# Performance work log

Hardware: AMD Instinct MI355X
Metric: run time of the kernel (lower is better)

Reference implementation:

```python
import jax, jax.numpy as jnp
import numpy as np

EPS = 0.01
H = 256
W = 256
C = 3
RADIUS_PX = 1.5          # splat radius in pixels
K_PPP = 8                # points_per_pixel
RAD_POW = 2
TAU = 1                  # accumulation_tau
WIN = 5                  # 5x5 candidate pixel window per point (covers radius 1.5)


def make_xyzs():
    # matches torch buffer: rows are (x, y, 1, 1) over flattened (H, W)
    xs = jnp.arange(W, dtype=jnp.float32)
    ys = jnp.arange(H, dtype=jnp.float32)
    X, Y = jnp.meshgrid(xs, ys)  # (H, W), X varies along width
    ones = jnp.ones_like(X)
    return jnp.stack([X, Y, ones, ones], 0).reshape(1, 4, H * W)


def project_pts(pred_pts, Kmat, K_inv, RT_cam1, RTinv_cam2):
    # pred_pts: (bs, 1, N) depths
    xyzs = make_xyzs()
    proj = xyzs * pred_pts                       # (bs, 4, N)
    proj = proj.at[:, 3, :].set(1.0)
    cam1 = jnp.einsum('bij,bjn->bin', K_inv, proj)
    wrld = jnp.einsum('bij,bjn->bin', RT_cam1, cam1)
    newc = jnp.einsum('bij,bjn->bin', RTinv_cam2, wrld)
    xy = jnp.einsum('bij,bjn->bin', Kmat, newc)
    z = xy[:, 2:3]
    mask = jnp.abs(z) < EPS
    zs = jnp.where(mask, EPS, z)
    sx = xy[:, 0:1] / zs / float(W - 1) * 2.0 - 1.0
    sy = xy[:, 1:2] / zs / float(H - 1) * 2.0 - 1.0
    sampler = jnp.concatenate([sx, sy, z], 1)    # (bs, 3, N)
    sampler = jnp.where(mask, -10.0, sampler)
    return sampler


def splat_one(pts, alpha_pts, feats):
    # pts: (N,3) ndc x,y + depth z; alpha_pts: (N,); feats: (C,N)
    N = pts.shape[0]
    x = (pts[:, 0] + 1.0) * 0.5 * (W - 1)        # ndc -> pixel coords
    y = (pts[:, 1] + 1.0) * 0.5 * (H - 1)
    z = pts[:, 2]
    radius_ndc = RADIUS_PX / float(W) * 2.0
    px0 = jnp.floor(x).astype(jnp.int32)
    py0 = jnp.floor(y).astype(jnp.int32)
    offs = jnp.arange(WIN, dtype=jnp.int32) - WIN // 2
    oy, ox = jnp.meshgrid(offs, offs, indexing='ij')
    oy = oy.reshape(-1)
    ox = ox.reshape(-1)                           # (25,)
    py = py0[:, None] + oy[None, :]               # (N, 25)
    px = px0[:, None] + ox[None, :]
    d2_pix = (px.astype(jnp.float32) - x[:, None]) ** 2 + (py.astype(jnp.float32) - y[:, None]) ** 2
    inb = (px >= 0) & (px < W) & (py >= 0) & (py < H)
    valid = inb & (d2_pix <= RADIUS_PX ** 2) & (z[:, None] > 0.0)
    d2_ndc = d2_pix * (2.0 / float(W)) ** 2
    dist_norm = d2_ndc / (radius_ndc ** RAD_POW)
    a = (1.0 - jnp.sqrt(jnp.clip(dist_norm, 1e-3, 1.0))) ** TAU
    a = a * alpha_pts[:, None]
    a = jnp.where(valid, a, 0.0)
    pix = jnp.where(valid, py * W + px, H * W)    # invalid -> dump segment
    M = N * WIN * WIN
    pixf = pix.reshape(M)
    zf = jnp.broadcast_to(z[:, None], pix.shape).reshape(M)
    af = a.reshape(M)
    ptid = jnp.broadcast_to(jnp.arange(N, dtype=jnp.int32)[:, None], pix.shape).reshape(M)
    # depth-ordered z-buffer: sort by (pixel, z), keep first K per pixel
    order = jnp.lexsort((zf, pixf))
    pixs = pixf[order]
    as_ = af[order]
    ids = ptid[order]
    first = jnp.searchsorted(pixs, pixs, side='left')
    rank = jnp.arange(M) - first
    keep = (rank < K_PPP) & (pixs < H * W)
    slot = jnp.where(keep, pixs * K_PPP + rank, H * W * K_PPP)
    alpha_buf = jnp.zeros(H * W * K_PPP + 1, jnp.float32).at[slot].set(as_)[:-1].reshape(H * W, K_PPP)
    idx_buf = jnp.full(H * W * K_PPP + 1, -1, jnp.int32).at[slot].set(ids)[:-1].reshape(H * W, K_PPP)
    feat = feats[:, jnp.clip(idx_buf, 0)]         # (C, HW, K)
    feat = jnp.where(idx_buf[None] >= 0, feat, 0.0)
    # front-to-back alpha composite
    one_m = 1.0 - alpha_buf
    t_exc = jnp.concatenate([jnp.ones((H * W, 1), jnp.float32), jnp.cumprod(one_m, axis=1)[:, :-1]], axis=1)
    wgt = alpha_buf * t_exc                       # (HW, K)
    out = jnp.einsum('chk,hk->ch', feat, wgt)
    return out.reshape(C, H, W)


def setup_inputs() -> dict:
    key = jax.random.key(0)
    k1, k2, k3 = jax.random.split(key, 3)
    bs = 2
    src = jax.random.normal(k1, (bs, C, H, W), jnp.float32)
    pred_pts = jax.random.uniform(k2, (bs, 1, H, W), jnp.float32) * 7.0 + 1.0  # depths in [1, 8]
    alphas = jax.random.uniform(k3, (bs, 1, H, W), jnp.float32)
    f = float(W)
    Kn = np.array([[f, 0, W / 2.0, 0], [0, f, H / 2.0, 0], [0, 0, 1, 0], [0, 0, 0, 1]], np.float32)
    K_inv_n = np.linalg.inv(Kn).astype(np.float32)
    th = 0.05
    R = np.array([[np.cos(th), 0, np.sin(th), 0.1], [0, 1, 0, 0], [-np.sin(th), 0, np.cos(th), 0], [0, 0, 0, 1]], np.float32)
    I4 = np.eye(4, dtype=np.float32)
    tile = lambda m: jnp.asarray(np.broadcast_to(m, (bs, 4, 4)).copy())
    return {
        'alphas': alphas, 'src': src, 'pred_pts': pred_pts,
        'K': tile(Kn), 'K_inv': tile(K_inv_n),
        'RT_cam1': tile(I4), 'RTinv_cam1': tile(I4),
        'RT_cam2': tile(np.linalg.inv(R).astype(np.float32)), 'RTinv_cam2': tile(R),
    }


def reference(alphas, src, pred_pts, K, K_inv, RT_cam1, RTinv_cam1, RT_cam2, RTinv_cam2):
    bs, c = src.shape[0], src.shape[1]
    pred = pred_pts.reshape(bs, 1, -1)
    srcf = src.reshape(bs, c, -1)
    al = alphas.reshape(bs, -1)
    sampler = project_pts(pred, K, K_inv, RT_cam1, RTinv_cam2)
    pts = jnp.transpose(sampler, (0, 2, 1))       # (bs, N, 3)
    return jax.vmap(splat_one)(pts, al, srcf)     # (bs, C, H, W)
```

## Files before the change

### kernel.cpp

```cpp
#include <hip/hip_runtime.h>
#include <math.h>

#define HH 256
#define WW 256
#define NPIX (HH*WW)
#define GW (WW+4)
#define GH (HH+4)
#define NC (GW*GH)
#define CHUNK 256
#define NCHUNKS ((NC + CHUNK - 1) / CHUNK)
#define EPSF 0.01f
#define GATE 2.24997f

__device__ __forceinline__ float dot4(const float* M, int i, float a0, float a1, float a2, float a3) {
    float s = __fmul_rn(M[i*4+0], a0);
    s = __fadd_rn(s, __fmul_rn(M[i*4+1], a1));
    s = __fadd_rn(s, __fmul_rn(M[i*4+2], a2));
    s = __fadd_rn(s, __fmul_rn(M[i*4+3], a3));
    return s;
}

__global__ void proj_kernel(const float* __restrict__ pred, const float* __restrict__ alphas,
                            const float* __restrict__ Kinv, const float* __restrict__ RT1,
                            const float* __restrict__ RTi2, const float* __restrict__ Km,
                            float4* __restrict__ pts, int* __restrict__ counts) {
    int b = blockIdx.y;
    int n = blockIdx.x * blockDim.x + threadIdx.x;
    __shared__ float Ms[4][16];
    int t = threadIdx.x;
    if (t < 64) {
        const float* srcs[4] = {Kinv, RT1, RTi2, Km};
        Ms[t >> 4][t & 15] = srcs[t >> 4][b*16 + (t & 15)];
    }
    __syncthreads();
    const float* KIs = Ms[0];
    const float* R1s = Ms[1];
    const float* R2s = Ms[2];
    const float* Ks  = Ms[3];

    float d = pred[b*NPIX + n];
    float X = (float)(n & (WW-1));
    float Y = (float)(n >> 8);
    float p0 = __fmul_rn(X, d);
    float p1 = __fmul_rn(Y, d);
    float p2 = d;
    float p3 = 1.0f;
    float c0 = dot4(KIs, 0, p0, p1, p2, p3);
    float c1 = dot4(KIs, 1, p0, p1, p2, p3);
    float c2 = dot4(KIs, 2, p0, p1, p2, p3);
    float c3 = dot4(KIs, 3, p0, p1, p2, p3);
    float w0 = dot4(R1s, 0, c0, c1, c2, c3);
    float w1 = dot4(R1s, 1, c0, c1, c2, c3);
    float w2 = dot4(R1s, 2, c0, c1, c2, c3);
    float w3 = dot4(R1s, 3, c0, c1, c2, c3);
    float q0 = dot4(R2s, 0, w0, w1, w2, w3);
    float q1 = dot4(R2s, 1, w0, w1, w2, w3);
    float q2 = dot4(R2s, 2, w0, w1, w2, w3);
    float q3 = dot4(R2s, 3, w0, w1, w2, w3);
    float xy0 = dot4(Ks, 0, q0, q1, q2, q3);
    float xy1 = dot4(Ks, 1, q0, q1, q2, q3);
    float z   = dot4(Ks, 2, q0, q1, q2, q3);

    bool mask = fabsf(z) < EPSF;
    float zs = mask ? EPSF : z;
    float tx = __fdiv_rn(xy0, zs);
    tx = __fdiv_rn(tx, 255.0f);
    tx = __fmul_rn(tx, 2.0f);
    float sx = __fsub_rn(tx, 1.0f);
    float ty = __fdiv_rn(xy1, zs);
    ty = __fdiv_rn(ty, 255.0f);
    ty = __fmul_rn(ty, 2.0f);
    float sy = __fsub_rn(ty, 1.0f);
    float sxm = mask ? -10.0f : sx;
    float sym = mask ? -10.0f : sy;
    float zo  = mask ? -10.0f : z;
    float x = __fmul_rn(__fmul_rn(__fadd_rn(sxm, 1.0f), 0.5f), 255.0f);
    float y = __fmul_rn(__fmul_rn(__fadd_rn(sym, 1.0f), 0.5f), 255.0f);

    float al = alphas[b*NPIX + n];
    pts[(size_t)b*NPIX + n] = make_float4(x, y, zo, al);

    if (zo > 0.0f) {
        float fx = floorf(x), fy = floorf(y);
        if (fx >= -2.0f && fx <= (float)(WW+1) && fy >= -2.0f && fy <= (float)(HH+1)) {
            int cx = (int)fx + 2, cy = (int)fy + 2;
            atomicAdd(&counts[(size_t)b*NC + cy*GW + cx], 1);
        }
    }
}


__global__ void scan_part(const int* __restrict__ counts, int* __restrict__ starts,
                          int* __restrict__ bsum) {
    int b = blockIdx.y;
    int chunk = blockIdx.x;
    int tid = threadIdx.x;
    int i = chunk*CHUNK + tid;
    int v = (i < NC) ? counts[(size_t)b*NC + i] : 0;
    __shared__ int sh[CHUNK];
    sh[tid] = v;
    __syncthreads();
    for (int off = 1; off < CHUNK; off <<= 1) {
        int t = (tid >= off) ? sh[tid - off] : 0;
        __syncthreads();
        sh[tid] += t;
        __syncthreads();
    }
    if (i < NC) starts[(size_t)b*(NC+1) + i] = sh[tid] - v;
    if (tid == CHUNK-1) bsum[b*NCHUNKS + chunk] = sh[tid];
}

__global__ void scan_bsum(const int* __restrict__ bsum, int* __restrict__ bsx,
                          int* __restrict__ starts) {
    int b = blockIdx.x;
    int tid = threadIdx.x;
    int v = (tid < NCHUNKS) ? bsum[b*NCHUNKS + tid] : 0;
    __shared__ int sh[512];
    sh[tid] = v;
    __syncthreads();
    for (int off = 1; off < 512; off <<= 1) {
        int t = (tid >= off) ? sh[tid - off] : 0;
        __syncthreads();
        sh[tid] += t;
        __syncthreads();
    }
    if (tid < NCHUNKS) bsx[b*NCHUNKS + tid] = sh[tid] - v;
    if (tid == 511) starts[(size_t)b*(NC+1) + NC] = sh[tid];
}

__global__ void scan_add(int* __restrict__ starts, const int* __restrict__ bsx,
                         int* __restrict__ cursor) {
    int b = blockIdx.y;
    int chunk = blockIdx.x;
    int tid = threadIdx.x;
    int i = chunk*CHUNK + tid;
    if (i < NC) {
        int s = starts[(size_t)b*(NC+1) + i] + bsx[b*NCHUNKS + chunk];
        starts[(size_t)b*(NC+1) + i] = s;
        cursor[(size_t)b*NC + i] = s;
    }
}

__global__ void scatter_kernel(const float4* __restrict__ pts, int* __restrict__ cursor,
                               int* __restrict__ bin_ids) {
    int b = blockIdx.y;
    int n = blockIdx.x * blockDim.x + threadIdx.x;
    float4 r = pts[(size_t)b*NPIX + n];
    if (r.z > 0.0f) {
        float fx = floorf(r.x), fy = floorf(r.y);
        if (fx >= -2.0f && fx <= (float)(WW+1) && fy >= -2.0f && fy <= (float)(HH+1)) {
            int cx = (int)fx + 2, cy = (int)fy + 2;
            int pos = atomicAdd(&cursor[(size_t)b*NC + cy*GW + cx], 1);
            bin_ids[(size_t)b*NPIX + pos] = n;
        }
    }
}

__global__ void gather_kernel(const float4* __restrict__ pts, const int* __restrict__ starts,
                              const int* __restrict__ bin_ids, const float* __restrict__ src,
                              float* __restrict__ out) {
    int b = blockIdx.y;
    int p = blockIdx.x * blockDim.x + threadIdx.x;
    int px = p & (WW-1);
    int py = p >> 8;
    const int* st = starts + (size_t)b*(NC+1);
    const int* ids = bin_ids + (size_t)b*NPIX;
    const float4* P = pts + (size_t)b*NPIX;

    float zz[8]; int ii[8]; float aa[8];
#pragma unroll
    for (int k = 0; k < 8; ++k) { zz[k] = INFINITY; ii[k] = 0x7fffffff; aa[k] = 0.f; }

    float fpx = (float)px, fpy = (float)py;
    for (int cy = py; cy <= py + 4; ++cy) {
        int base = cy*GW + px;
        int s = st[base];
        int e = st[base + 5];
        for (int j = s; j < e; ++j) {
            int n = ids[j];
            float4 r = P[n];
            float dx = __fsub_rn(fpx, r.x);
            float dy = __fsub_rn(fpy, r.y);
            float d2 = __fadd_rn(__fmul_rn(dx, dx), __fmul_rn(dy, dy));
            if (!(d2 <= GATE)) continue;
            float dn = __fdiv_rn(d2, 2.25f);
            dn = fminf(fmaxf(dn, 0.001f), 1.0f);
            float ta = __fmul_rn(__fsub_rn(1.0f, sqrtf(dn)), r.w);
            float tz = r.z; int tn = n;
#pragma unroll
            for (int k = 0; k < 8; ++k) {
                bool lt = (tz < zz[k]) || (tz == zz[k] && tn < ii[k]);
                float oz = zz[k]; int oi = ii[k]; float oa = aa[k];
                zz[k] = lt ? tz : oz;  ii[k] = lt ? tn : oi;  aa[k] = lt ? ta : oa;
                tz = lt ? oz : tz;     tn = lt ? oi : tn;     ta = lt ? oa : ta;
            }
        }
    }

    float T = 1.0f, c0 = 0.f, c1 = 0.f, c2 = 0.f;
#pragma unroll
    for (int k = 0; k < 8; ++k) {
        int n = ii[k];
        if (n != 0x7fffffff) {
            float wgt = __fmul_rn(aa[k], T);
            c0 = __fadd_rn(c0, __fmul_rn(wgt, src[((size_t)b*3 + 0)*NPIX + n]));
            c1 = __fadd_rn(c1, __fmul_rn(wgt, src[((size_t)b*3 + 1)*NPIX + n]));
            c2 = __fadd_rn(c2, __fmul_rn(wgt, src[((size_t)b*3 + 2)*NPIX + n]));
            T = __fmul_rn(T, __fsub_rn(1.0f, aa[k]));
        }
    }
    out[((size_t)b*3 + 0)*NPIX + p] = c0;
    out[((size_t)b*3 + 1)*NPIX + p] = c1;
    out[((size_t)b*3 + 2)*NPIX + p] = c2;
}

extern "C" void kernel_launch(void* const* d_in, const int* in_sizes, int n_in,
                              void* d_out, int out_size, void* d_ws, size_t ws_size,
                              hipStream_t stream) {
    const float* alphas = (const float*)d_in[0];
    const float* src    = (const float*)d_in[1];
    const float* pred   = (const float*)d_in[2];
    const float* Kmat   = (const float*)d_in[3];
    const float* Kinv   = (const float*)d_in[4];
    const float* RT1    = (const float*)d_in[5];
    const float* RTinv2 = (const float*)d_in[8];
    float* out = (float*)d_out;

    int bs = in_sizes[0] / NPIX;

    char* w = (char*)d_ws;
    size_t need = 0;
    float4* pts   = (float4*)(w);                 need += (size_t)bs*NPIX*sizeof(float4);
    int*    cnts  = (int*)(w + need);             need += (size_t)bs*NC*sizeof(int);
    int*    strts = (int*)(w + need);             need += (size_t)bs*(NC+1)*sizeof(int);
    int*    curs  = (int*)(w + need);             need += (size_t)bs*NC*sizeof(int);
    int*    bids  = (int*)(w + need);             need += (size_t)bs*NPIX*sizeof(int);
    int*    bsum  = (int*)(w + need);             need += (size_t)bs*NCHUNKS*sizeof(int);
    int*    bsx   = (int*)(w + need);             need += (size_t)bs*NCHUNKS*sizeof(int);
    if (ws_size < need) return;

    hipMemsetAsync(cnts, 0, (size_t)bs*NC*sizeof(int), stream);
    proj_kernel<<<dim3(NPIX/256, bs), 256, 0, stream>>>(pred, alphas, Kinv, RT1, RTinv2, Kmat, pts, cnts);
    scan_part<<<dim3(NCHUNKS, bs), CHUNK, 0, stream>>>(cnts, strts, bsum);
    scan_bsum<<<bs, 512, 0, stream>>>(bsum, bsx, strts);
    scan_add<<<dim3(NCHUNKS, bs), CHUNK, 0, stream>>>(strts, bsx, curs);
    scatter_kernel<<<dim3(NPIX/256, bs), 256, 0, stream>>>(pts, curs, bids);
    gather_kernel<<<dim3(NPIX/256, bs), 256, 0, stream>>>(pts, strts, bids, src, out);
}
```

Measured before the change: 65.71 us.

## Store binned point data contiguously, pack RGB, fold block-sum scan into scan_add

The scatter pass now writes each point's float4 (x,y,z,alpha) into bin order next to its id, so the gather loop reads contiguous records instead of making an indirect random load per candidate. The id is loaded only after the distance gate passes. Source colours are repacked into a float4 per point, so the final blend needs one load instead of three strided loads. The separate block-sum scan kernel is removed, and each scan_add block reduces the preceding chunk sums itself, which saves one launch at the cost of redundant reductions and extra workspace writes.

```diff
diff --git a/kernel.cpp b/kernel.cpp
--- a/kernel.cpp
+++ b/kernel.cpp
@@ -89,7 +89,6 @@
     }
 }
 
-
 __global__ void scan_part(const int* __restrict__ counts, int* __restrict__ starts,
                           int* __restrict__ bsum) {
     int b = blockIdx.y;
@@ -110,62 +109,63 @@
     if (tid == CHUNK-1) bsum[b*NCHUNKS + chunk] = sh[tid];
 }
 
-__global__ void scan_bsum(const int* __restrict__ bsum, int* __restrict__ bsx,
-                          int* __restrict__ starts) {
-    int b = blockIdx.x;
-    int tid = threadIdx.x;
-    int v = (tid < NCHUNKS) ? bsum[b*NCHUNKS + tid] : 0;
-    __shared__ int sh[512];
-    sh[tid] = v;
-    __syncthreads();
-    for (int off = 1; off < 512; off <<= 1) {
-        int t = (tid >= off) ? sh[tid - off] : 0;
-        __syncthreads();
-        sh[tid] += t;
-        __syncthreads();
-    }
-    if (tid < NCHUNKS) bsx[b*NCHUNKS + tid] = sh[tid] - v;
-    if (tid == 511) starts[(size_t)b*(NC+1) + NC] = sh[tid];
-}
-
-__global__ void scan_add(int* __restrict__ starts, const int* __restrict__ bsx,
+__global__ void scan_add(int* __restrict__ starts, const int* __restrict__ bsum,
                          int* __restrict__ cursor) {
     int b = blockIdx.y;
     int chunk = blockIdx.x;
     int tid = threadIdx.x;
+    __shared__ int sh[CHUNK];
+    int v0 = (tid < chunk) ? bsum[b*NCHUNKS + tid] : 0;
+    int i2 = tid + CHUNK;
+    int v1 = (i2 < NCHUNKS && i2 < chunk) ? bsum[b*NCHUNKS + i2] : 0;
+    sh[tid] = v0 + v1;
+    __syncthreads();
+    for (int off = CHUNK/2; off > 0; off >>= 1) {
+        if (tid < off) sh[tid] += sh[tid + off];
+        __syncthreads();
+    }
+    int offset = sh[0];
     int i = chunk*CHUNK + tid;
     if (i < NC) {
-        int s = starts[(size_t)b*(NC+1) + i] + bsx[b*NCHUNKS + chunk];
+        int s = starts[(size_t)b*(NC+1) + i] + offset;
         starts[(size_t)b*(NC+1) + i] = s;
         cursor[(size_t)b*NC + i] = s;
     }
+    if (chunk == NCHUNKS-1 && tid == 0)
+        starts[(size_t)b*(NC+1) + NC] = offset + bsum[b*NCHUNKS + NCHUNKS-1];
 }
 
 __global__ void scatter_kernel(const float4* __restrict__ pts, int* __restrict__ cursor,
-                               int* __restrict__ bin_ids) {
+                               float4* __restrict__ bpts, int* __restrict__ bids,
+                               const float* __restrict__ src, float4* __restrict__ rgb) {
     int b = blockIdx.y;
     int n = blockIdx.x * blockDim.x + threadIdx.x;
     float4 r = pts[(size_t)b*NPIX + n];
+    float f0 = src[((size_t)b*3 + 0)*NPIX + n];
+    float f1 = src[((size_t)b*3 + 1)*NPIX + n];
+    float f2 = src[((size_t)b*3 + 2)*NPIX + n];
+    rgb[(size_t)b*NPIX + n] = make_float4(f0, f1, f2, 0.f);
     if (r.z > 0.0f) {
         float fx = floorf(r.x), fy = floorf(r.y);
         if (fx >= -2.0f && fx <= (float)(WW+1) && fy >= -2.0f && fy <= (float)(HH+1)) {
             int cx = (int)fx + 2, cy = (int)fy + 2;
             int pos = atomicAdd(&cursor[(size_t)b*NC + cy*GW + cx], 1);
-            bin_ids[(size_t)b*NPIX + pos] = n;
-        }
-    }
-}
-
-__global__ void gather_kernel(const float4* __restrict__ pts, const int* __restrict__ starts,
-                              const int* __restrict__ bin_ids, const float* __restrict__ src,
+            bpts[(size_t)b*NPIX + pos] = r;
+            bids[(size_t)b*NPIX + pos] = n;
+        }
+    }
+}
+
+__global__ void gather_kernel(const float4* __restrict__ bpts, const int* __restrict__ starts,
+                              const int* __restrict__ bids, const float4* __restrict__ rgb,
                               float* __restrict__ out) {
     int b = blockIdx.y;
     int p = blockIdx.x * blockDim.x + threadIdx.x;
     int px = p & (WW-1);
     int py = p >> 8;
     const int* st = starts + (size_t)b*(NC+1);
-    const int* ids = bin_ids + (size_t)b*NPIX;
-    const float4* P = pts + (size_t)b*NPIX;
+    const int* ids = bids + (size_t)b*NPIX;
+    const float4* B = bpts + (size_t)b*NPIX;
 
     float zz[8]; int ii[8]; float aa[8];
 #pragma unroll
@@ -177,12 +177,12 @@
         int s = st[base];
         int e = st[base + 5];
         for (int j = s; j < e; ++j) {
-            int n = ids[j];
-            float4 r = P[n];
+            float4 r = B[j];
             float dx = __fsub_rn(fpx, r.x);
             float dy = __fsub_rn(fpy, r.y);
             float d2 = __fadd_rn(__fmul_rn(dx, dx), __fmul_rn(dy, dy));
             if (!(d2 <= GATE)) continue;
+            int n = ids[j];
             float dn = __fdiv_rn(d2, 2.25f);
             dn = fminf(fmaxf(dn, 0.001f), 1.0f);
             float ta = __fmul_rn(__fsub_rn(1.0f, sqrtf(dn)), r.w);
@@ -197,15 +197,17 @@
         }
     }
 
+    const float4* F = rgb + (size_t)b*NPIX;
     float T = 1.0f, c0 = 0.f, c1 = 0.f, c2 = 0.f;
 #pragma unroll
     for (int k = 0; k < 8; ++k) {
         int n = ii[k];
         if (n != 0x7fffffff) {
             float wgt = __fmul_rn(aa[k], T);
-            c0 = __fadd_rn(c0, __fmul_rn(wgt, src[((size_t)b*3 + 0)*NPIX + n]));
-            c1 = __fadd_rn(c1, __fmul_rn(wgt, src[((size_t)b*3 + 1)*NPIX + n]));
-            c2 = __fadd_rn(c2, __fmul_rn(wgt, src[((size_t)b*3 + 2)*NPIX + n]));
+            float4 f = F[n];
+            c0 = __fadd_rn(c0, __fmul_rn(wgt, f.x));
+            c1 = __fadd_rn(c1, __fmul_rn(wgt, f.y));
+            c2 = __fadd_rn(c2, __fmul_rn(wgt, f.z));
             T = __fmul_rn(T, __fsub_rn(1.0f, aa[k]));
         }
     }
@@ -231,19 +233,19 @@
     char* w = (char*)d_ws;
     size_t need = 0;
     float4* pts   = (float4*)(w);                 need += (size_t)bs*NPIX*sizeof(float4);
+    float4* bpts  = (float4*)(w + need);          need += (size_t)bs*NPIX*sizeof(float4);
+    float4* rgb   = (float4*)(w + need);          need += (size_t)bs*NPIX*sizeof(float4);
     int*    cnts  = (int*)(w + need);             need += (size_t)bs*NC*sizeof(int);
     int*    strts = (int*)(w + need);             need += (size_t)bs*(NC+1)*sizeof(int);
     int*    curs  = (int*)(w + need);             need += (size_t)bs*NC*sizeof(int);
     int*    bids  = (int*)(w + need);             need += (size_t)bs*NPIX*sizeof(int);
     int*    bsum  = (int*)(w + need);             need += (size_t)bs*NCHUNKS*sizeof(int);
-    int*    bsx   = (int*)(w + need);             need += (size_t)bs*NCHUNKS*sizeof(int);
     if (ws_size < need) return;
 
     hipMemsetAsync(cnts, 0, (size_t)bs*NC*sizeof(int), stream);
     proj_kernel<<<dim3(NPIX/256, bs), 256, 0, stream>>>(pred, alphas, Kinv, RT1, RTinv2, Kmat, pts, cnts);
     scan_part<<<dim3(NCHUNKS, bs), CHUNK, 0, stream>>>(cnts, strts, bsum);
-    scan_bsum<<<bs, 512, 0, stream>>>(bsum, bsx, strts);
-    scan_add<<<dim3(NCHUNKS, bs), CHUNK, 0, stream>>>(strts, bsx, curs);
-    scatter_kernel<<<dim3(NPIX/256, bs), 256, 0, stream>>>(pts, curs, bids);
-    gather_kernel<<<dim3(NPIX/256, bs), 256, 0, stream>>>(pts, strts, bids, src, out);
-}
+    scan_add<<<dim3(NCHUNKS, bs), CHUNK, 0, stream>>>(strts, bsum, curs);
+    scatter_kernel<<<dim3(NPIX/256, bs), 256, 0, stream>>>(pts, curs, bpts, bids, src, rgb);
+    gather_kernel<<<dim3(NPIX/256, bs), 256, 0, stream>>>(bpts, strts, bids, rgb, out);
+}
```

After: 63.01 us. 1.04x faster.
